# Kernel tuning notes

Hardware: AMD Instinct MI355X
Metric: run time of the kernel (lower is better)

The kernel has to match this reference:

```python
import jax, jax.numpy as jnp
import numpy as np

HEADS = 4
DIM_HEAD = 4


def setup_inputs() -> dict:
    key = jax.random.key(0)
    k1, k2, k3, k4 = jax.random.split(key, 4)
    B, C, H, W = 4, 64, 64, 64
    hidden = HEADS * DIM_HEAD  # 16
    x = jax.random.normal(k1, (B, C, H, W), dtype=jnp.float32)
    # 1x1 convs are just channel matmuls; store squeezed kernels
    w_qkv = jax.random.normal(k2, (3 * hidden, C), dtype=jnp.float32) * 0.05
    w_out = jax.random.normal(k3, (C, hidden), dtype=jnp.float32) * 0.05
    b_out = jax.random.normal(k4, (C,), dtype=jnp.float32) * 0.05
    return {"x": x, "w_qkv": w_qkv, "w_out": w_out, "b_out": b_out}


def reference(x, w_qkv, w_out, b_out):
    B, C, H, W = x.shape
    n = H * W
    scale = DIM_HEAD ** -0.5
    # to_qkv: 1x1 conv, no bias -> [B, 3*hidden, n]
    qkv = jnp.einsum('oc,bcn->bon', w_qkv, x.reshape(B, C, n))
    q, k, v = jnp.split(qkv, 3, axis=1)
    # 'b (h d) n -> b h d n'
    def to_heads(t):
        return t.reshape(B, HEADS, DIM_HEAD, n)
    q, k, v = to_heads(q) * scale, to_heads(k), to_heads(v)
    sim = jnp.einsum('bhdi,bhdj->bhij', q, k)           # [B,H,n,n]
    attn = jax.nn.softmax(sim, axis=-1)
    out = jnp.einsum('bhij,bhdj->bhid', attn, v)        # [B,H,n,d]
    # 'b h n d -> b (h d) h w'
    out = out.transpose(0, 1, 3, 2).reshape(B, HEADS * DIM_HEAD, H, W)
    # to_out: 1x1 conv with bias
    y = jnp.einsum('oc,bchw->bohw', w_out, out) + b_out[None, :, None, None]
    return y
```

## Files before the change

### kernel.cpp

```cpp
#include <hip/hip_runtime.h>
#include <hip/hip_bf16.h>

#define N_POS 4096
#define BH 16
#define JS 4

typedef float f32x16 __attribute__((ext_vector_type(16)));
typedef short bf16x8 __attribute__((ext_vector_type(8)));

#define QSCALE (0.5f * 1.44269504088896f)

__device__ __forceinline__ float fexp2(float x) {
#if __has_builtin(__builtin_amdgcn_exp2f)
    return __builtin_amdgcn_exp2f(x);
#else
    return exp2f(x);
#endif
}

__device__ __forceinline__ unsigned int bfbits(float f) {
    __hip_bfloat16 h = __float2bfloat16(f);
    return (unsigned int)*reinterpret_cast<unsigned short*>(&h);
}
__device__ __forceinline__ float bff32(unsigned int u) {
    unsigned int w = u << 16;
    float f;
    __builtin_memcpy(&f, &w, 4);
    return f;
}
__device__ __forceinline__ unsigned int pk2(unsigned int lo, unsigned int hi) {
    return lo | (hi << 16);
}

__global__ __launch_bounds__(256) void qkv_pack(const float* __restrict__ x,
                                                const float* __restrict__ w_qkv,
                                                uint4* __restrict__ qfrag,
                                                uint4* __restrict__ kfrag,
                                                unsigned short* __restrict__ vfrag) {
    int blk = blockIdx.x;
    int role = blk >> 8;
    int bh = (blk >> 4) & 15;
    int chunk = blk & 15;
    int b = bh >> 2, h = bh & 3;
    int i = chunk * 256 + threadIdx.x;

    const float* xb = x + ((size_t)b * 64) * N_POS + i;
    const float* wr = w_qkv + (role * 16 + h * 4) * 64;

    float a[4] = {0, 0, 0, 0};
#pragma unroll 8
    for (int c = 0; c < 64; ++c) {
        float xv = xb[(size_t)c * N_POS];
#pragma unroll
        for (int d = 0; d < 4; ++d)
            a[d] = fmaf(wr[d * 64 + c], xv, a[d]);
    }

    int it = i >> 5, il = i & 31;
    size_t base = ((size_t)(bh * 128 + it) * 2) * 32 + il;

    if (role == 0) {
        unsigned int qh[4], ql[4];
#pragma unroll
        for (int d = 0; d < 4; ++d) {
            float qs = a[d] * QSCALE;
            qh[d] = bfbits(qs);
            ql[d] = bfbits(qs - bff32(qh[d]));
        }
        qfrag[base]      = make_uint4(pk2(qh[0], qh[1]), pk2(qh[2], qh[3]),
                                      pk2(ql[0], ql[1]), pk2(ql[2], ql[3]));
        qfrag[base + 32] = make_uint4(pk2(qh[0], qh[1]), pk2(qh[2], qh[3]), 0u, 0u);
    } else if (role == 1) {
        unsigned int kh[4], kl[4];
#pragma unroll
        for (int d = 0; d < 4; ++d) {
            kh[d] = bfbits(a[d]);
            kl[d] = bfbits(a[d] - bff32(kh[d]));
        }
        kfrag[base]      = make_uint4(pk2(kh[0], kh[1]), pk2(kh[2], kh[3]),
                                      pk2(kh[0], kh[1]), pk2(kh[2], kh[3]));
        kfrag[base + 32] = make_uint4(pk2(kl[0], kl[1]), pk2(kl[2], kl[3]), 0u, 0u);
    } else {
        int step = i >> 4, vh = (i >> 3) & 1, e = i & 7;
        size_t ventry = ((size_t)(bh * 256 + step) * 2 + vh) * 5;
#pragma unroll
        for (int d = 0; d < 4; ++d)
            vfrag[(ventry + d) * 8 + e] = (unsigned short)bfbits(a[d]);
        if (e == 0)
            reinterpret_cast<uint4*>(vfrag)[ventry + 4] =
                make_uint4(0x3F803F80u, 0x3F803F80u, 0x3F803F80u, 0x3F803F80u);
    }
}

__global__ __launch_bounds__(256, 4) void attn_mfma(const uint4* __restrict__ qfrag,
                                                    const uint4* __restrict__ kfrag,
                                                    const uint4* __restrict__ vfrag,
                                                    float* __restrict__ pacc,
                                                    float* __restrict__ pl) {
    constexpr int JT = 128 / JS;
    int wave = threadIdx.x >> 6;
    int lane = threadIdx.x & 63;
    int half = lane >> 5, c = lane & 31;
    int blk = blockIdx.x;
    int js = blk & (JS - 1);
    int itg = (blk / JS) & 31;
    int bh = blk / (JS * 32);
    int it = itg * 4 + wave;

    uint4 qf_u = qfrag[((size_t)(bh * 128 + it) * 2 + half) * 32 + c];
    bf16x8 qf = __builtin_bit_cast(bf16x8, qf_u);

    const uint4* kp = kfrag + (size_t)bh * 128 * 64 + (size_t)js * JT * 64
                    + (size_t)half * 32 + c;
    int vcol = c < 4 ? c : 4;
    const uint4* vp = vfrag + (size_t)bh * 2560 + (size_t)js * JT * 20
                    + half * 5 + vcol;

    f32x16 acc, zc;
#pragma unroll
    for (int r = 0; r < 16; ++r) { acc[r] = 0.f; zc[r] = 0.f; }

    uint4 kf_n = kp[0];
    uint4 v0_c = vp[0], v1_c = vp[10];
    f32x16 s_cur = __builtin_amdgcn_mfma_f32_32x32x16_bf16(
        __builtin_bit_cast(bf16x8, kf_n), qf, zc, 0, 0, 0);
    kf_n = kp[64];

#pragma unroll 2
    for (int jj = 0; jj < JT; ++jj) {
        int j2 = (jj + 2 < JT) ? jj + 2 : JT - 1;
        int j1 = (jj + 1 < JT) ? jj + 1 : JT - 1;
        uint4 kf_p = kp[j2 * 64];
        uint4 v0_n = vp[(2 * j1) * 10];
        uint4 v1_n = vp[(2 * j1 + 1) * 10];

        f32x16 s_next = __builtin_amdgcn_mfma_f32_32x32x16_bf16(
            __builtin_bit_cast(bf16x8, kf_n), qf, zc, 0, 0, 0);

        unsigned int t[8];
#pragma unroll
        for (int eo = 0; eo < 8; ++eo) {
            float plo = fexp2(s_cur[2 * eo]);
            float phi = fexp2(s_cur[2 * eo + 1]);
            unsigned int r_;
            asm("v_cvt_pk_bf16_f32 %0, %1, %2" : "=v"(r_) : "v"(plo), "v"(phi));
            t[eo] = r_;
        }
        asm("v_permlane32_swap_b32 %0, %1" : "+v"(t[0]), "+v"(t[2]));
        asm("v_permlane32_swap_b32 %0, %1" : "+v"(t[1]), "+v"(t[3]));
        asm("v_permlane32_swap_b32 %0, %1" : "+v"(t[4]), "+v"(t[6]));
        asm("v_permlane32_swap_b32 %0, %1" : "+v"(t[5]), "+v"(t[7]));
        bf16x8 pa0 = __builtin_bit_cast(bf16x8, make_uint4(t[0], t[1], t[2], t[3]));
        bf16x8 pa1 = __builtin_bit_cast(bf16x8, make_uint4(t[4], t[5], t[6], t[7]));

        __builtin_amdgcn_s_setprio(1);
        acc = __builtin_amdgcn_mfma_f32_32x32x16_bf16(
            pa0, __builtin_bit_cast(bf16x8, v0_c), acc, 0, 0, 0);
        acc = __builtin_amdgcn_mfma_f32_32x32x16_bf16(
            pa1, __builtin_bit_cast(bf16x8, v1_c), acc, 0, 0, 0);
        __builtin_amdgcn_s_setprio(0);

        s_cur = s_next;
        kf_n = kf_p;
        v0_c = v0_n;
        v1_c = v1_n;
    }

    size_t pbase = (size_t)(js * BH + bh) * N_POS + it * 32;
    if (c < 4) {
#pragma unroll
        for (int r = 0; r < 16; ++r) {
            int row = (r & 3) + 8 * (r >> 2) + 4 * half;
            pacc[(pbase + row) * 4 + c] = acc[r];
        }
    } else if (c == 4) {
#pragma unroll
        for (int r = 0; r < 16; ++r) {
            int row = (r & 3) + 8 * (r >> 2) + 4 * half;
            pl[pbase + row] = acc[r];
        }
    }
}

__global__ __launch_bounds__(256) void out_proj(const float4* __restrict__ pacc,
                                                const float* __restrict__ pl,
                                                const float* __restrict__ w_out,
                                                const float* __restrict__ b_out,
                                                float* __restrict__ y) {
    int t = blockIdx.x * 256 + threadIdx.x;
    int i  = t & 4095;
    int cg = (t >> 12) & 15;
    int b  = t >> 16;

    float of[16];
#pragma unroll
    for (int h = 0; h < 4; ++h) {
        int bh = b * 4 + h;
        float sx = 0.f, sy = 0.f, sz = 0.f, sw = 0.f, l = 0.f;
#pragma unroll
        for (int js = 0; js < JS; ++js) {
            size_t idx = (size_t)(js * BH + bh) * N_POS + i;
            float4 a = pacc[idx];
            sx += a.x; sy += a.y; sz += a.z; sw += a.w;
            l += pl[idx];
        }
        float inv = 1.0f / l;
        of[h * 4 + 0] = sx * inv;
        of[h * 4 + 1] = sy * inv;
        of[h * 4 + 2] = sz * inv;
        of[h * 4 + 3] = sw * inv;
    }

    float* yb = y + ((size_t)b * 64 + cg * 4) * N_POS + i;
#pragma unroll
    for (int cc = 0; cc < 4; ++cc) {
        int ch = cg * 4 + cc;
        const float* wr = w_out + ch * 16;
        float s = b_out[ch];
#pragma unroll
        for (int u = 0; u < 16; ++u) s = fmaf(wr[u], of[u], s);
        yb[(size_t)cc * N_POS] = s;
    }
}

extern "C" void kernel_launch(void* const* d_in, const int* in_sizes, int n_in,
                              void* d_out, int out_size, void* d_ws, size_t ws_size,
                              hipStream_t stream) {
    const float* x     = (const float*)d_in[0];
    const float* w_qkv = (const float*)d_in[1];
    const float* w_out = (const float*)d_in[2];
    const float* b_out = (const float*)d_in[3];
    float* y = (float*)d_out;

    char* w = (char*)d_ws;
    uint4*          qfrag = (uint4*)(w);
    uint4*          kfrag = (uint4*)(w + 2097152);
    unsigned short* vfrag = (unsigned short*)(w + 4194304);
    float*          pacc  = (float*)(w + 5242880);
    float*          pl    = (float*)(w + 5242880 + (size_t)JS * 1048576);

    qkv_pack<<<3 * 256, 256, 0, stream>>>(x, w_qkv, qfrag, kfrag, vfrag);
    attn_mfma<<<BH * 32 * JS, 256, 0, stream>>>(qfrag, kfrag, (const uint4*)vfrag,
                                                pacc, pl);
    out_proj<<<1024, 256, 0, stream>>>((const float4*)pacc, pl, w_out, b_out, y);
}
```

Baseline: 53.50 us.

## Process two query tiles per wave to reuse K/V fragments and halve grid

Each wave now handles two 32-row query tiles, sharing each loaded K fragment and V fragments between two QK^T MFMAs and two PV accumulations. The grid is halved accordingly. The old software pipelining of the score MFMA (computing the next S while exponentiating the current one) is replaced by in-iteration interleaving of the two independent tiles. This cuts K/V load traffic per unit of work and gives the scheduler independent MFMA/exp chains, at the cost of more registers and fewer blocks.

```diff
diff --git a/kernel.cpp b/kernel.cpp
--- a/kernel.cpp
+++ b/kernel.cpp
@@ -103,12 +103,15 @@
     int half = lane >> 5, c = lane & 31;
     int blk = blockIdx.x;
     int js = blk & (JS - 1);
-    int itg = (blk / JS) & 31;
-    int bh = blk / (JS * 32);
-    int it = itg * 4 + wave;
-
-    uint4 qf_u = qfrag[((size_t)(bh * 128 + it) * 2 + half) * 32 + c];
-    bf16x8 qf = __builtin_bit_cast(bf16x8, qf_u);
+    int itg = (blk / JS) & 15;
+    int bh = blk / (JS * 16);
+    int it0 = itg * 8 + wave * 2;
+    int it1 = it0 + 1;
+
+    bf16x8 qfA = __builtin_bit_cast(bf16x8,
+        qfrag[((size_t)(bh * 128 + it0) * 2 + half) * 32 + c]);
+    bf16x8 qfB = __builtin_bit_cast(bf16x8,
+        qfrag[((size_t)(bh * 128 + it1) * 2 + half) * 32 + c]);
 
     const uint4* kp = kfrag + (size_t)bh * 128 * 64 + (size_t)js * JT * 64
                     + (size_t)half * 32 + c;
@@ -116,15 +119,13 @@
     const uint4* vp = vfrag + (size_t)bh * 2560 + (size_t)js * JT * 20
                     + half * 5 + vcol;
 
-    f32x16 acc, zc;
-#pragma unroll
-    for (int r = 0; r < 16; ++r) { acc[r] = 0.f; zc[r] = 0.f; }
-
-    uint4 kf_n = kp[0];
+    f32x16 accA, accB, zc;
+#pragma unroll
+    for (int r = 0; r < 16; ++r) { accA[r] = 0.f; accB[r] = 0.f; zc[r] = 0.f; }
+
+    uint4 kf_c = kp[0];
+    uint4 kf_n = kp[64];
     uint4 v0_c = vp[0], v1_c = vp[10];
-    f32x16 s_cur = __builtin_amdgcn_mfma_f32_32x32x16_bf16(
-        __builtin_bit_cast(bf16x8, kf_n), qf, zc, 0, 0, 0);
-    kf_n = kp[64];
 
 #pragma unroll 2
     for (int jj = 0; jj < JT; ++jj) {
@@ -134,50 +135,75 @@
         uint4 v0_n = vp[(2 * j1) * 10];
         uint4 v1_n = vp[(2 * j1 + 1) * 10];
 
-        f32x16 s_next = __builtin_amdgcn_mfma_f32_32x32x16_bf16(
-            __builtin_bit_cast(bf16x8, kf_n), qf, zc, 0, 0, 0);
-
-        unsigned int t[8];
-#pragma unroll
-        for (int eo = 0; eo < 8; ++eo) {
-            float plo = fexp2(s_cur[2 * eo]);
-            float phi = fexp2(s_cur[2 * eo + 1]);
-            unsigned int r_;
-            asm("v_cvt_pk_bf16_f32 %0, %1, %2" : "=v"(r_) : "v"(plo), "v"(phi));
-            t[eo] = r_;
-        }
-        asm("v_permlane32_swap_b32 %0, %1" : "+v"(t[0]), "+v"(t[2]));
-        asm("v_permlane32_swap_b32 %0, %1" : "+v"(t[1]), "+v"(t[3]));
-        asm("v_permlane32_swap_b32 %0, %1" : "+v"(t[4]), "+v"(t[6]));
-        asm("v_permlane32_swap_b32 %0, %1" : "+v"(t[5]), "+v"(t[7]));
-        bf16x8 pa0 = __builtin_bit_cast(bf16x8, make_uint4(t[0], t[1], t[2], t[3]));
-        bf16x8 pa1 = __builtin_bit_cast(bf16x8, make_uint4(t[4], t[5], t[6], t[7]));
-
-        __builtin_amdgcn_s_setprio(1);
-        acc = __builtin_amdgcn_mfma_f32_32x32x16_bf16(
-            pa0, __builtin_bit_cast(bf16x8, v0_c), acc, 0, 0, 0);
-        acc = __builtin_amdgcn_mfma_f32_32x32x16_bf16(
-            pa1, __builtin_bit_cast(bf16x8, v1_c), acc, 0, 0, 0);
-        __builtin_amdgcn_s_setprio(0);
-
-        s_cur = s_next;
-        kf_n = kf_p;
-        v0_c = v0_n;
-        v1_c = v1_n;
-    }
-
-    size_t pbase = (size_t)(js * BH + bh) * N_POS + it * 32;
+        bf16x8 kf = __builtin_bit_cast(bf16x8, kf_c);
+        f32x16 sA = __builtin_amdgcn_mfma_f32_32x32x16_bf16(kf, qfA, zc, 0, 0, 0);
+        f32x16 sB = __builtin_amdgcn_mfma_f32_32x32x16_bf16(kf, qfB, zc, 0, 0, 0);
+
+        bf16x8 v0 = __builtin_bit_cast(bf16x8, v0_c);
+        bf16x8 v1 = __builtin_bit_cast(bf16x8, v1_c);
+
+        {
+            unsigned int t[8];
+#pragma unroll
+            for (int eo = 0; eo < 8; ++eo) {
+                float plo = fexp2(sA[2 * eo]);
+                float phi = fexp2(sA[2 * eo + 1]);
+                unsigned int r_;
+                asm("v_cvt_pk_bf16_f32 %0, %1, %2" : "=v"(r_) : "v"(plo), "v"(phi));
+                t[eo] = r_;
+            }
+            asm("v_permlane32_swap_b32 %0, %1" : "+v"(t[0]), "+v"(t[2]));
+            asm("v_permlane32_swap_b32 %0, %1" : "+v"(t[1]), "+v"(t[3]));
+            asm("v_permlane32_swap_b32 %0, %1" : "+v"(t[4]), "+v"(t[6]));
+            asm("v_permlane32_swap_b32 %0, %1" : "+v"(t[5]), "+v"(t[7]));
+            bf16x8 pa0 = __builtin_bit_cast(bf16x8, make_uint4(t[0], t[1], t[2], t[3]));
+            bf16x8 pa1 = __builtin_bit_cast(bf16x8, make_uint4(t[4], t[5], t[6], t[7]));
+            __builtin_amdgcn_s_setprio(1);
+            accA = __builtin_amdgcn_mfma_f32_32x32x16_bf16(pa0, v0, accA, 0, 0, 0);
+            accA = __builtin_amdgcn_mfma_f32_32x32x16_bf16(pa1, v1, accA, 0, 0, 0);
+            __builtin_amdgcn_s_setprio(0);
+        }
+        {
+            unsigned int t[8];
+#pragma unroll
+            for (int eo = 0; eo < 8; ++eo) {
+                float plo = fexp2(sB[2 * eo]);
+                float phi = fexp2(sB[2 * eo + 1]);
+                unsigned int r_;
+                asm("v_cvt_pk_bf16_f32 %0, %1, %2" : "=v"(r_) : "v"(plo), "v"(phi));
+                t[eo] = r_;
+            }
+            asm("v_permlane32_swap_b32 %0, %1" : "+v"(t[0]), "+v"(t[2]));
+            asm("v_permlane32_swap_b32 %0, %1" : "+v"(t[1]), "+v"(t[3]));
+            asm("v_permlane32_swap_b32 %0, %1" : "+v"(t[4]), "+v"(t[6]));
+            asm("v_permlane32_swap_b32 %0, %1" : "+v"(t[5]), "+v"(t[7]));
+            bf16x8 pa0 = __builtin_bit_cast(bf16x8, make_uint4(t[0], t[1], t[2], t[3]));
+            bf16x8 pa1 = __builtin_bit_cast(bf16x8, make_uint4(t[4], t[5], t[6], t[7]));
+            __builtin_amdgcn_s_setprio(1);
+            accB = __builtin_amdgcn_mfma_f32_32x32x16_bf16(pa0, v0, accB, 0, 0, 0);
+            accB = __builtin_amdgcn_mfma_f32_32x32x16_bf16(pa1, v1, accB, 0, 0, 0);
+            __builtin_amdgcn_s_setprio(0);
+        }
+
+        kf_c = kf_n; kf_n = kf_p;
+        v0_c = v0_n; v1_c = v1_n;
+    }
+
+    size_t pbase0 = (size_t)(js * BH + bh) * N_POS + it0 * 32;
+    size_t pbase1 = pbase0 + 32;
     if (c < 4) {
 #pragma unroll
         for (int r = 0; r < 16; ++r) {
             int row = (r & 3) + 8 * (r >> 2) + 4 * half;
-            pacc[(pbase + row) * 4 + c] = acc[r];
+            pacc[(pbase0 + row) * 4 + c] = accA[r];
+            pacc[(pbase1 + row) * 4 + c] = accB[r];
         }
     } else if (c == 4) {
 #pragma unroll
         for (int r = 0; r < 16; ++r) {
             int row = (r & 3) + 8 * (r >> 2) + 4 * half;
-            pl[pbase + row] = acc[r];
+            pl[pbase0 + row] = accA[r];
+            pl[pbase1 + row] = accB[r];
         }
     }
 }
@@ -240,7 +266,7 @@
     float*          pl    = (float*)(w + 5242880 + (size_t)JS * 1048576);
 
     qkv_pack<<<3 * 256, 256, 0, stream>>>(x, w_qkv, qfrag, kfrag, vfrag);
-    attn_mfma<<<BH * 32 * JS, 256, 0, stream>>>(qfrag, kfrag, (const uint4*)vfrag,
+    attn_mfma<<<BH * 16 * JS, 256, 0, stream>>>(qfrag, kfrag, (const uint4*)vfrag,
                                                 pacc, pl);
     out_proj<<<1024, 256, 0, stream>>>((const float4*)pacc, pl, w_out, b_out, y);
 }
```

Measured after the change: 52.60 us (median of 2 runs). Within noise of the previous version (-1.7%).
